# Optimization experiments

Hardware: AMD Instinct MI355X
Metric: run time of the kernel (lower is better)

## Reference

```python
import jax, jax.numpy as jnp
import numpy as np

D_MODEL = 1024
NUM_HEADS = 16
HEAD_DIM = D_MODEL // NUM_HEADS


def setup_inputs() -> dict:
    key = jax.random.key(0)
    k1, k2, k3, k4, k5 = jax.random.split(key, 5)
    scale = 1.0 / np.sqrt(D_MODEL)
    x = jax.random.normal(k1, (2, 2048, D_MODEL), dtype=jnp.float32)
    Wqkv = jax.random.uniform(k2, (D_MODEL, 3 * D_MODEL), jnp.float32, -scale, scale)
    bqkv = jax.random.uniform(k3, (3 * D_MODEL,), jnp.float32, -scale, scale)
    Wout = jax.random.uniform(k4, (D_MODEL, D_MODEL), jnp.float32, -scale, scale)
    bout = jax.random.uniform(k5, (D_MODEL,), jnp.float32, -scale, scale)
    return {"x": x, "Wqkv": Wqkv, "bqkv": bqkv, "Wout": Wout, "bout": bout}


def reference(x, Wqkv, bqkv, Wout, bout):
    B, S, _ = x.shape
    qkv = x @ Wqkv + bqkv                                   # [B, S, 3*D]
    # reshape to [B, S, H, 3*head_dim] then to [B, H, S, 3*head_dim]
    qkv = qkv.reshape(B, S, NUM_HEADS, 3 * HEAD_DIM).transpose(0, 2, 1, 3)
    q, k, v = jnp.split(qkv, 3, axis=-1)                    # each [B, H, S, hd]
    scaled = jnp.einsum("bhqd,bhkd->bhqk", q, k) / jnp.sqrt(jnp.float32(HEAD_DIM))
    attn = jax.nn.softmax(scaled, axis=-1)                  # [B, H, S, S]
    values = jnp.einsum("bhqk,bhkd->bhqd", attn, v)         # [B, H, S, hd]
    values = values.transpose(0, 2, 1, 3).reshape(B, S, D_MODEL)
    return values @ Wout + bout
```

## Files before the change

kernel.cpp:

```cpp
#include <hip/hip_runtime.h>


typedef __attribute__((ext_vector_type(8)))  short short8;
typedef __attribute__((ext_vector_type(4)))  short short4v;
typedef __attribute__((ext_vector_type(8)))  float float8;
typedef __attribute__((ext_vector_type(4)))  float f32x4;
typedef __attribute__((ext_vector_type(16))) float f32x16;
typedef __attribute__((ext_vector_type(4)))  int   int4v;

#define D_MODEL 1024
#define NHEAD   16
#define HD      64
#define SEQ     2048
#define N3      (3*D_MODEL)
#define MB      (1024*1024)

static __device__ __forceinline__ float bf2f(short s) {
    unsigned u = ((unsigned)(unsigned short)s) << 16;
    return __builtin_bit_cast(float, u);
}
static __device__ __forceinline__ short f2bf(float f) {
    unsigned u = __builtin_bit_cast(unsigned, f);
    u = (u + 0x7fff + ((u >> 16) & 1)) >> 16;
    return (short)u;
}
static __device__ __forceinline__ unsigned cvtpk(float a, float b) {
    unsigned r;
    asm("v_cvt_pk_bf16_f32 %0, %1, %2" : "=v"(r) : "v"(a), "v"(b));
    return r;
}
#define PLSWAP(a, b) asm("v_permlane32_swap_b32 %0, %1" : "+v"(a), "+v"(b))

static __device__ __forceinline__ void gl16(const short* g, short* l) {
    __builtin_amdgcn_global_load_lds(
        (const __attribute__((address_space(1))) unsigned int*)g,
        (__attribute__((address_space(3))) unsigned int*)l, 16, 0, 0);
}

__global__ __launch_bounds__(256) void prep(
    const float* __restrict__ x, const float* __restrict__ Wqkv,
    const float* __restrict__ Wout,
    short* __restrict__ Xh, short* __restrict__ Xl,
    short* __restrict__ Wh, short* __restrict__ Wl,
    short* __restrict__ Woh, short* __restrict__ Wol)
{
    __shared__ float tile[32][33];
    const int bid = blockIdx.x;
    const int tid = threadIdx.x;

    if (bid < 2048) {
        const int i = (bid * 256 + tid) * 8;
        const float8 v = *(const float8*)&x[i];
        short8 h, l;
#pragma unroll
        for (int j = 0; j < 8; ++j) {
            h[j] = f2bf(v[j]);
            l[j] = f2bf(v[j] - bf2f(h[j]));
        }
        *(short8*)&Xh[i] = h;
        *(short8*)&Xl[i] = l;
        return;
    }

    const float* in; short *hi, *lo; int K, N, bx, by;
    if (bid < 5120) {
        const int b2 = bid - 2048;
        in = Wqkv; hi = Wh; lo = Wl; K = D_MODEL; N = N3;
        bx = b2 % 96; by = b2 / 96;
    } else {
        const int b3 = bid - 5120;
        in = Wout; hi = Woh; lo = Wol; K = D_MODEL; N = D_MODEL;
        bx = b3 & 31; by = b3 >> 5;
    }
    const int n0 = bx * 32, k0 = by * 32;
    const int tx = tid & 31, ty = tid >> 5;
#pragma unroll
    for (int i = 0; i < 4; ++i)
        tile[ty + 8*i][tx] = in[(k0 + ty + 8*i) * N + (n0 + tx)];
    __syncthreads();
#pragma unroll
    for (int i = 0; i < 4; ++i) {
        const float v  = tile[tx][ty + 8*i];
        const short vh = f2bf(v);
        const short vl = f2bf(v - bf2f(vh));
        const int idx  = (n0 + ty + 8*i) * K + (k0 + tx);
        hi[idx] = vh;
        lo[idx] = vl;
    }
}

#define QBUF_SH 20480
#define OFF_AL  4096
#define OFF_BH  8192
#define OFF_BL  14336

__global__ __launch_bounds__(512, 4) void qkv_gemm8(
    const short* __restrict__ Xh, const short* __restrict__ Xl,
    const short* __restrict__ Bh, const short* __restrict__ Bl,
    const float* __restrict__ bias,
    short* __restrict__ Qo, short* __restrict__ Ko, short* __restrict__ Vt)
{
    __shared__ __attribute__((aligned(16))) short smem[2 * QBUF_SH];

    const int tid  = threadIdx.x;
    const int wave = tid >> 6, lane = tid & 63;
    const int q4 = lane >> 4, l16 = lane & 15;
    const int wr = wave >> 2, wc = wave & 3;
    const int csw = (q4 ^ ((l16 ^ (l16 >> 2)) & 3)) * 8;

    const int flat = blockIdx.x;
    const int sw = (flat & 7) * 64 + (flat >> 3);
    const int mt = sw & 31, nt = sw >> 5;
    const int m0 = mt * 128, n0 = nt * 192;

    const short* srcp[5];
#pragma unroll
    for (int j = 0; j < 5; ++j) {
        const int id = j * 512 + tid;
        int r; const short* mat; int row0;
        if (id < 512)       { r = id >> 2;          mat = Xh; row0 = m0; }
        else if (id < 1024) { r = (id - 512) >> 2;  mat = Xl; row0 = m0; }
        else if (id < 1792) { r = (id - 1024) >> 2; mat = Bh; row0 = n0; }
        else                { r = (id - 1792) >> 2; mat = Bl; row0 = n0; }
        const int cg = (id & 3) ^ ((r ^ (r >> 2)) & 3);
        srcp[j] = &mat[(size_t)(row0 + r) * D_MODEL + cg * 8];
    }

    auto stage = [&](int b) {
#pragma unroll
        for (int j = 0; j < 5; ++j) {
            gl16(srcp[j], smem + b * QBUF_SH + (j * 512 + tid) * 8);
            srcp[j] += 32;
        }
    };

    f32x4 acc[4][3];
#pragma unroll
    for (int i = 0; i < 4; ++i)
#pragma unroll
        for (int j = 0; j < 3; ++j) acc[i][j] = (f32x4){0.f, 0.f, 0.f, 0.f};

    stage(0);
    asm volatile("s_waitcnt vmcnt(0)" ::: "memory");
    __builtin_amdgcn_s_barrier();

    for (int t = 0; t < 32; ++t) {
        const int cur = t & 1;
        const short* base = smem + cur * QBUF_SH;
        const short* Ah_s = base;
        const short* Al_s = base + OFF_AL;
        const short* Bh_s = base + OFF_BH;
        const short* Bl_s = base + OFF_BL;

        short8 bhf[3], blf[3], a0h[2], a0l[2];
#pragma unroll
        for (int n = 0; n < 3; ++n) {
            const int rb = (wc * 48 + n * 16 + l16) * 32 + csw;
            bhf[n] = *(const short8*)(Bh_s + rb);
            blf[n] = *(const short8*)(Bl_s + rb);
        }
#pragma unroll
        for (int ti = 0; ti < 2; ++ti) {
            const int ra = (wr * 64 + ti * 16 + l16) * 32 + csw;
            a0h[ti] = *(const short8*)(Ah_s + ra);
            a0l[ti] = *(const short8*)(Al_s + ra);
        }
        if (t < 31) stage(cur ^ 1);
        __builtin_amdgcn_s_barrier();
        asm volatile("s_waitcnt lgkmcnt(0)" ::: "memory");
        __builtin_amdgcn_sched_barrier(0);
        short8 a1h[2], a1l[2];
#pragma unroll
        for (int ti = 0; ti < 2; ++ti) {
            const int ra = (wr * 64 + (2 + ti) * 16 + l16) * 32 + csw;
            a1h[ti] = *(const short8*)(Ah_s + ra);
            a1l[ti] = *(const short8*)(Al_s + ra);
        }
        __builtin_amdgcn_sched_barrier(0);
        __builtin_amdgcn_s_setprio(1);
#pragma unroll
        for (int ti = 0; ti < 2; ++ti)
#pragma unroll
            for (int n = 0; n < 3; ++n) {
                acc[ti][n] = __builtin_amdgcn_mfma_f32_16x16x32_bf16(a0h[ti], bhf[n], acc[ti][n], 0, 0, 0);
                acc[ti][n] = __builtin_amdgcn_mfma_f32_16x16x32_bf16(a0h[ti], blf[n], acc[ti][n], 0, 0, 0);
                acc[ti][n] = __builtin_amdgcn_mfma_f32_16x16x32_bf16(a0l[ti], bhf[n], acc[ti][n], 0, 0, 0);
            }
        __builtin_amdgcn_s_setprio(0);
        __builtin_amdgcn_s_barrier();

        asm volatile("s_waitcnt lgkmcnt(0)" ::: "memory");
        __builtin_amdgcn_sched_barrier(0);
        __builtin_amdgcn_s_setprio(1);
#pragma unroll
        for (int ti = 0; ti < 2; ++ti)
#pragma unroll
            for (int n = 0; n < 3; ++n) {
                acc[2+ti][n] = __builtin_amdgcn_mfma_f32_16x16x32_bf16(a1h[ti], bhf[n], acc[2+ti][n], 0, 0, 0);
                acc[2+ti][n] = __builtin_amdgcn_mfma_f32_16x16x32_bf16(a1h[ti], blf[n], acc[2+ti][n], 0, 0, 0);
                acc[2+ti][n] = __builtin_amdgcn_mfma_f32_16x16x32_bf16(a1l[ti], bhf[n], acc[2+ti][n], 0, 0, 0);
            }
        __builtin_amdgcn_s_setprio(0);
        asm volatile("s_waitcnt vmcnt(0)" ::: "memory");
        __builtin_amdgcn_s_barrier();
    }

    const float SCALE_Q = 0.125f * 1.4426950408889634f;
#pragma unroll
    for (int tj = 0; tj < 3; ++tj) {
        const int jj = wc * 48 + tj * 16 + l16;
        const int n  = nt * 192 + jj;
        const float bv = bias[n];
#pragma unroll
        for (int ti = 0; ti < 4; ++ti) {
            const int mb = m0 + wr * 64 + ti * 16 + q4 * 4;
            const int b = mb >> 11;
            const int s = mb & 2047;
            const int bh_ = b * NHEAD + nt;
            if (jj >= 128) {
                short4v v4;
#pragma unroll
                for (int r = 0; r < 4; ++r) v4[r] = f2bf(acc[ti][tj][r] + bv);
                *(short4v*)&Vt[(bh_ * HD + (jj - 128)) * SEQ + s] = v4;
            } else if (jj < 64) {
#pragma unroll
                for (int r = 0; r < 4; ++r)
                    Qo[(bh_ * SEQ + s + r) * HD + jj] = f2bf((acc[ti][tj][r] + bv) * SCALE_Q);
            } else {
#pragma unroll
                for (int r = 0; r < 4; ++r)
                    Ko[(bh_ * SEQ + s + r) * HD + (jj - 64)] = f2bf(acc[ti][tj][r] + bv);
            }
        }
    }
}

__global__ __launch_bounds__(256, 2) void attn_tscore(
    const short* __restrict__ Q, const short* __restrict__ K,
    const short* __restrict__ Vt,
    float* __restrict__ Opart, float2* __restrict__ Ml)
{
    __shared__ __attribute__((aligned(16))) char smem[36864];
    short (*Ks)[72] = (short(*)[72])smem;
    short (*Vs)[72] = (short(*)[72])(smem + 18432);

    const int bh  = blockIdx.x;
    const int qb  = blockIdx.y;
    const int kvz = blockIdx.z;

    const short* Qp  = Q  + (size_t)bh * SEQ * HD;
    const short* Kp  = K  + (size_t)bh * SEQ * HD + (size_t)kvz * 1024 * HD;
    const short* Vtp = Vt + (size_t)bh * HD * SEQ + (size_t)kvz * 1024;

    const int tid  = threadIdx.x;
    const int wave = tid >> 6, lane = tid & 63;
    const int l5 = lane & 31, hf = lane >> 5;
    const int q0w = qb * 128 + wave * 32;

    short8 qf[4];
#pragma unroll
    for (int c = 0; c < 4; ++c)
        qf[c] = *(const short8*)&Qp[(q0w + l5) * HD + c * 16 + hf * 8];

    f32x16 oacc0 = (f32x16)(0.f), oacc1 = (f32x16)(0.f);
    float m = -1.0e30f, l = 0.f;

    const int sr = tid >> 2;
    const int sc = (tid & 3) * 16;

    short8 kr0 = *(const short8*)&Kp[sr * HD + sc];
    short8 kr1 = *(const short8*)&Kp[sr * HD + sc + 8];
    short8 vr0 = *(const short8*)&Vtp[sr * SEQ + sc];
    short8 vr1 = *(const short8*)&Vtp[sr * SEQ + sc + 8];
    *(short8*)&Ks[sr][sc]     = kr0;
    *(short8*)&Ks[sr][sc + 8] = kr1;
    *(short8*)&Vs[sr][sc]     = vr0;
    *(short8*)&Vs[sr][sc + 8] = vr1;
    __syncthreads();

    for (int kc = 0; kc < 16; ++kc) {
        const int buf = (kc & 1) << 6;

        if (kc < 15) {
            const int nkb = (kc + 1) << 6;
            kr0 = *(const short8*)&Kp[(nkb + sr) * HD + sc];
            kr1 = *(const short8*)&Kp[(nkb + sr) * HD + sc + 8];
            vr0 = *(const short8*)&Vtp[sr * SEQ + nkb + sc];
            vr1 = *(const short8*)&Vtp[sr * SEQ + nkb + sc + 8];
        }

        f32x16 s0 = (f32x16)(0.f), s1 = (f32x16)(0.f);
#pragma unroll
        for (int c = 0; c < 4; ++c) {
            const short8 ka0 = *(const short8*)&Ks[buf + l5][c * 16 + hf * 8];
            const short8 ka1 = *(const short8*)&Ks[buf + 32 + l5][c * 16 + hf * 8];
            s0 = __builtin_amdgcn_mfma_f32_32x32x16_bf16(ka0, qf[c], s0, 0, 0, 0);
            s1 = __builtin_amdgcn_mfma_f32_32x32x16_bf16(ka1, qf[c], s1, 0, 0, 0);
        }

        float t[8];
#pragma unroll
        for (int i = 0; i < 8; ++i)
            t[i] = fmaxf(fmaxf(s0[i], s0[i + 8]), fmaxf(s1[i], s1[i + 8]));
        float pmax = fmaxf(fmaxf(fmaxf(t[0], t[1]), fmaxf(t[2], t[3])),
                           fmaxf(fmaxf(t[4], t[5]), fmaxf(t[6], t[7])));
        pmax = fmaxf(pmax, __shfl_xor(pmax, 32, 64));

        if (!__all(pmax - m <= 8.0f)) {
            const float mnew  = fmaxf(m, pmax);
            const float alpha = exp2f(m - mnew);
#pragma unroll
            for (int i = 0; i < 16; ++i) { oacc0[i] *= alpha; oacc1[i] *= alpha; }
            l *= alpha;
            m = mnew;
        }

        float p0[16], p1[16];
#pragma unroll
        for (int i = 0; i < 16; ++i) { p0[i] = exp2f(s0[i] - m); p1[i] = exp2f(s1[i] - m); }
        float sa = 0.f, sb = 0.f, sc_ = 0.f, sd = 0.f;
#pragma unroll
        for (int i = 0; i < 4; ++i) {
            sa += p0[i] + p0[i + 8];
            sb += p0[i + 4] + p0[i + 12];
            sc_ += p1[i] + p1[i + 8];
            sd += p1[i + 4] + p1[i + 12];
        }
        float rs = (sa + sb) + (sc_ + sd);
        rs += __shfl_xor(rs, 32, 64);
        l += rs;

        unsigned u0 = cvtpk(p0[0],  p0[1]),  u1 = cvtpk(p0[2],  p0[3]);
        unsigned u2 = cvtpk(p0[4],  p0[5]),  u3 = cvtpk(p0[6],  p0[7]);
        unsigned u4 = cvtpk(p0[8],  p0[9]),  u5 = cvtpk(p0[10], p0[11]);
        unsigned u6 = cvtpk(p0[12], p0[13]), u7 = cvtpk(p0[14], p0[15]);
        unsigned w0 = cvtpk(p1[0],  p1[1]),  w1 = cvtpk(p1[2],  p1[3]);
        unsigned w2 = cvtpk(p1[4],  p1[5]),  w3 = cvtpk(p1[6],  p1[7]);
        unsigned w4 = cvtpk(p1[8],  p1[9]),  w5 = cvtpk(p1[10], p1[11]);
        unsigned w6 = cvtpk(p1[12], p1[13]), w7 = cvtpk(p1[14], p1[15]);
        PLSWAP(u0, u2); PLSWAP(u1, u3); PLSWAP(u4, u6); PLSWAP(u5, u7);
        PLSWAP(w0, w2); PLSWAP(w1, w3); PLSWAP(w4, w6); PLSWAP(w5, w7);
        int4v pb0 = (int4v){ (int)u0, (int)u1, (int)u2, (int)u3 };
        int4v pb1 = (int4v){ (int)u4, (int)u5, (int)u6, (int)u7 };
        int4v pb2 = (int4v){ (int)w0, (int)w1, (int)w2, (int)w3 };
        int4v pb3 = (int4v){ (int)w4, (int)w5, (int)w6, (int)w7 };
        const short8 pbf0 = __builtin_bit_cast(short8, pb0);
        const short8 pbf1 = __builtin_bit_cast(short8, pb1);
        const short8 pbf2 = __builtin_bit_cast(short8, pb2);
        const short8 pbf3 = __builtin_bit_cast(short8, pb3);

        {
            const short8 va0 = *(const short8*)&Vs[buf + l5][hf * 8];
            const short8 va1 = *(const short8*)&Vs[buf + l5][16 + hf * 8];
            const short8 va2 = *(const short8*)&Vs[buf + l5][32 + hf * 8];
            const short8 va3 = *(const short8*)&Vs[buf + l5][48 + hf * 8];
            oacc0 = __builtin_amdgcn_mfma_f32_32x32x16_bf16(va0, pbf0, oacc0, 0, 0, 0);
            oacc0 = __builtin_amdgcn_mfma_f32_32x32x16_bf16(va1, pbf1, oacc0, 0, 0, 0);
            oacc0 = __builtin_amdgcn_mfma_f32_32x32x16_bf16(va2, pbf2, oacc0, 0, 0, 0);
            oacc0 = __builtin_amdgcn_mfma_f32_32x32x16_bf16(va3, pbf3, oacc0, 0, 0, 0);
            const short8 vb0 = *(const short8*)&Vs[buf + 32 + l5][hf * 8];
            const short8 vb1 = *(const short8*)&Vs[buf + 32 + l5][16 + hf * 8];
            const short8 vb2 = *(const short8*)&Vs[buf + 32 + l5][32 + hf * 8];
            const short8 vb3 = *(const short8*)&Vs[buf + 32 + l5][48 + hf * 8];
            oacc1 = __builtin_amdgcn_mfma_f32_32x32x16_bf16(vb0, pbf0, oacc1, 0, 0, 0);
            oacc1 = __builtin_amdgcn_mfma_f32_32x32x16_bf16(vb1, pbf1, oacc1, 0, 0, 0);
            oacc1 = __builtin_amdgcn_mfma_f32_32x32x16_bf16(vb2, pbf2, oacc1, 0, 0, 0);
            oacc1 = __builtin_amdgcn_mfma_f32_32x32x16_bf16(vb3, pbf3, oacc1, 0, 0, 0);
        }

        if (kc < 15) {
            const int wb = ((kc + 1) & 1) << 6;
            *(short8*)&Ks[wb + sr][sc]     = kr0;
            *(short8*)&Ks[wb + sr][sc + 8] = kr1;
            *(short8*)&Vs[wb + sr][sc]     = vr0;
            *(short8*)&Vs[wb + sr][sc + 8] = vr1;
        }
        __syncthreads();
    }

    float* Op = Opart + ((((size_t)kvz * 32 + bh) * 16 + qb) * 4 + wave) * 2048;
#pragma unroll
    for (int r = 0; r < 4; ++r) {
        float4 v;
        v.x = oacc0[4*r]; v.y = oacc0[4*r+1]; v.z = oacc0[4*r+2]; v.w = oacc0[4*r+3];
        *(float4*)&Op[r * 256 + lane * 4] = v;
    }
#pragma unroll
    for (int r = 0; r < 4; ++r) {
        float4 v;
        v.x = oacc1[4*r]; v.y = oacc1[4*r+1]; v.z = oacc1[4*r+2]; v.w = oacc1[4*r+3];
        *(float4*)&Op[(4 + r) * 256 + lane * 4] = v;
    }
    if (hf == 0) {
        float2 mv; mv.x = m; mv.y = l;
        Ml[((size_t)kvz * 32 + bh) * 2048 + q0w + l5] = mv;
    }
}

__global__ __launch_bounds__(256) void attn_merge(
    const float* __restrict__ Opart, const float2* __restrict__ Ml,
    short* __restrict__ Ch, short* __restrict__ Cl)
{
    __shared__ float epi[4][32][68];
    const int tid = threadIdx.x, wave = tid >> 6, lane = tid & 63;
    const int l5 = lane & 31, hf = lane >> 5;
    const int task = blockIdx.x * 4 + wave;
    const int bh = task >> 6;
    const int qb = (task >> 2) & 15;
    const int wq = task & 3;
    const int bi = bh >> 4, hi_ = bh & 15;
    const int q0w = qb * 128 + wq * 32;

    const float2 v0 = Ml[(size_t)bh * 2048 + q0w + l5];
    const float2 v1 = Ml[((size_t)32 + bh) * 2048 + q0w + l5];
    const float M  = fmaxf(v0.x, v1.x);
    const float w0 = exp2f(v0.x - M), w1 = exp2f(v1.x - M);
    const float inv = 1.0f / (v0.y * w0 + v1.y * w1);
    const float f0 = w0 * inv, f1 = w1 * inv;

    const float* Op0 = Opart + (((size_t)bh * 16 + qb) * 4 + wq) * 2048;
    const float* Op1 = Opart + ((((size_t)32 + bh) * 16 + qb) * 4 + wq) * 2048;
    float o[32];
#pragma unroll
    for (int r = 0; r < 8; ++r) {
        const float4 a = *(const float4*)&Op0[r * 256 + lane * 4];
        const float4 b = *(const float4*)&Op1[r * 256 + lane * 4];
        o[4*r]   = a.x * f0 + b.x * f1;
        o[4*r+1] = a.y * f0 + b.y * f1;
        o[4*r+2] = a.z * f0 + b.z * f1;
        o[4*r+3] = a.w * f0 + b.w * f1;
    }
#pragma unroll
    for (int r = 0; r < 16; ++r) {
        const int d = (r & 3) + 8 * (r >> 2) + 4 * hf;
        epi[wave][l5][d]      = o[r];
        epi[wave][l5][32 + d] = o[16 + r];
    }
    __builtin_amdgcn_s_waitcnt(0);
#pragma unroll
    for (int pass = 0; pass < 8; ++pass) {
        const int row = pass * 4 + (lane >> 4);
        const int col = (lane & 15) * 4;
        const float4 v = *(const float4*)&epi[wave][row][col];
        const float ov[4] = {v.x, v.y, v.z, v.w};
        short4v hh, ll;
#pragma unroll
        for (int i = 0; i < 4; ++i) {
            hh[i] = f2bf(ov[i]);
            ll[i] = f2bf(ov[i] - bf2f(hh[i]));
        }
        const size_t co = ((size_t)(bi * SEQ + q0w + row)) * D_MODEL + hi_ * HD + col;
        *(short4v*)&Ch[co] = hh;
        *(short4v*)&Cl[co] = ll;
    }
}

__global__ __launch_bounds__(256) void out_gemm128(
    const short* __restrict__ Ah, const short* __restrict__ Al,
    const short* __restrict__ Bh, const short* __restrict__ Bl,
    const float* __restrict__ bias, float* __restrict__ out)
{
    __shared__ short AhS[128*32], AlS[128*32], BhS[128*32], BlS[128*32];

    const int tid  = threadIdx.x;
    const int wave = tid >> 6, lane = tid & 63;
    const int q4 = lane >> 4, l16 = lane & 15;
    const int m0 = blockIdx.y * 128, n0 = blockIdx.x * 128;
    const int rw = (wave & 1) * 64, cw = (wave >> 1) * 64;
    const int trow = tid >> 2;
    const int tcol = (((tid & 3) ^ ((trow ^ (trow >> 2)) & 3))) * 8;
    const int csw = (q4 ^ ((l16 ^ (l16 >> 2)) & 3)) * 8;

    f32x4 acc[4][4];
#pragma unroll
    for (int i = 0; i < 4; ++i)
#pragma unroll
        for (int j = 0; j < 4; ++j) acc[i][j] = (f32x4){0.f, 0.f, 0.f, 0.f};

    for (int kt = 0; kt < D_MODEL; kt += 32) {
        gl16(&Ah[(m0 + trow) * D_MODEL + kt + tcol],      AhS + tid * 8);
        gl16(&Ah[(m0 + 64 + trow) * D_MODEL + kt + tcol], AhS + 2048 + tid * 8);
        gl16(&Al[(m0 + trow) * D_MODEL + kt + tcol],      AlS + tid * 8);
        gl16(&Al[(m0 + 64 + trow) * D_MODEL + kt + tcol], AlS + 2048 + tid * 8);
        gl16(&Bh[(n0 + trow) * D_MODEL + kt + tcol],      BhS + tid * 8);
        gl16(&Bh[(n0 + 64 + trow) * D_MODEL + kt + tcol], BhS + 2048 + tid * 8);
        gl16(&Bl[(n0 + trow) * D_MODEL + kt + tcol],      BlS + tid * 8);
        gl16(&Bl[(n0 + 64 + trow) * D_MODEL + kt + tcol], BlS + 2048 + tid * 8);
        __syncthreads();

        short8 ah[4], al[4], bh[4], bl[4];
#pragma unroll
        for (int t = 0; t < 4; ++t) {
            const int ra = (rw + t * 16 + l16) * 32 + csw;
            const int rb = (cw + t * 16 + l16) * 32 + csw;
            ah[t] = *(const short8*)&AhS[ra];
            al[t] = *(const short8*)&AlS[ra];
            bh[t] = *(const short8*)&BhS[rb];
            bl[t] = *(const short8*)&BlS[rb];
        }
#pragma unroll
        for (int ti = 0; ti < 4; ++ti)
#pragma unroll
            for (int tj = 0; tj < 4; ++tj) {
                acc[ti][tj] = __builtin_amdgcn_mfma_f32_16x16x32_bf16(ah[ti], bh[tj], acc[ti][tj], 0, 0, 0);
                acc[ti][tj] = __builtin_amdgcn_mfma_f32_16x16x32_bf16(ah[ti], bl[tj], acc[ti][tj], 0, 0, 0);
                acc[ti][tj] = __builtin_amdgcn_mfma_f32_16x16x32_bf16(al[ti], bh[tj], acc[ti][tj], 0, 0, 0);
            }
        __syncthreads();
    }

#pragma unroll
    for (int tj = 0; tj < 4; ++tj) {
        const int n = n0 + cw + tj * 16 + l16;
        const float bv = bias[n];
#pragma unroll
        for (int ti = 0; ti < 4; ++ti) {
            const int mb = m0 + rw + ti * 16 + q4 * 4;
#pragma unroll
            for (int r = 0; r < 4; ++r)
                out[(mb + r) * D_MODEL + n] = acc[ti][tj][r] + bv;
        }
    }
}

extern "C" void kernel_launch(void* const* d_in, const int* in_sizes, int n_in,
                              void* d_out, int out_size, void* d_ws, size_t ws_size,
                              hipStream_t stream)
{
    const float* x    = (const float*)d_in[0];
    const float* Wqkv = (const float*)d_in[1];
    const float* bqkv = (const float*)d_in[2];
    const float* Wout = (const float*)d_in[3];
    const float* bout = (const float*)d_in[4];
    float* out = (float*)d_out;

    char* ws = (char*)d_ws;
    short*  Woh   = (short*)(ws);
    short*  Wol   = (short*)(ws +  2*MB);
    short*  Qb    = (short*)(ws +  4*MB);
    short*  Kb    = (short*)(ws + 12*MB);
    short*  Vtb   = (short*)(ws + 20*MB);
    float*  Opart = (float*)(ws + 28*MB);
    float2* Ml    = (float2*)(ws + 60*MB);
    short*  Ch    = (short*)(ws +  4*MB);
    short*  Cl    = (short*)(ws + 12*MB);
    short*  Xh    = (short*)(ws + 28*MB);
    short*  Xl    = (short*)(ws + 36*MB);
    short*  Wh    = (short*)(ws + 44*MB);
    short*  Wl    = (short*)(ws + 50*MB);

    prep<<<6144, 256, 0, stream>>>(x, Wqkv, Wout, Xh, Xl, Wh, Wl, Woh, Wol);
    qkv_gemm8<<<dim3(512), 512, 0, stream>>>(Xh, Xl, Wh, Wl, bqkv, Qb, Kb, Vtb);
    attn_tscore<<<dim3(32, 16, 2), 256, 0, stream>>>(Qb, Kb, Vtb, Opart, Ml);
    attn_merge<<<512, 256, 0, stream>>>(Opart, Ml, Ch, Cl);
    out_gemm128<<<dim3(8, 32), 256, 0, stream>>>(Ch, Cl, Woh, Wol, bout, out);
}
```

Before: 275.8 us.

## Triple-buffer QKV GEMM LDS staging with two-stage-ahead prefetch

The QKV projection GEMM moves from a double-buffered LDS ring to a triple-buffered one. Global loads are now issued two K-steps ahead, and the wait uses a partial vmcnt so one stage's loads can stay in flight. The mid-iteration barrier split of the A fragments is removed in favour of a single fragment load and one MFMA phase per step. LDS use grows to about 120 KB per block, so launch bounds drop from 4 to 2 blocks per CU, giving up occupancy for deeper latency hiding.

New measurement: 286.8 us. 4.0% more time.

```diff
diff --git a/kernel.cpp b/kernel.cpp
--- a/kernel.cpp
+++ b/kernel.cpp
@@ -94,13 +94,13 @@
 #define OFF_BH  8192
 #define OFF_BL  14336
 
-__global__ __launch_bounds__(512, 4) void qkv_gemm8(
+__global__ __launch_bounds__(512, 2) void qkv_gemm8(
     const short* __restrict__ Xh, const short* __restrict__ Xl,
     const short* __restrict__ Bh, const short* __restrict__ Bl,
     const float* __restrict__ bias,
     short* __restrict__ Qo, short* __restrict__ Ko, short* __restrict__ Vt)
 {
-    __shared__ __attribute__((aligned(16))) short smem[2 * QBUF_SH];
+    __shared__ __attribute__((aligned(16))) short smem[3 * QBUF_SH];
 
     const int tid  = threadIdx.x;
     const int wave = tid >> 6, lane = tid & 63;
@@ -141,18 +141,20 @@
         for (int j = 0; j < 3; ++j) acc[i][j] = (f32x4){0.f, 0.f, 0.f, 0.f};
 
     stage(0);
-    asm volatile("s_waitcnt vmcnt(0)" ::: "memory");
+    stage(1);
+    asm volatile("s_waitcnt vmcnt(5)" ::: "memory");
     __builtin_amdgcn_s_barrier();
 
     for (int t = 0; t < 32; ++t) {
-        const int cur = t & 1;
-        const short* base = smem + cur * QBUF_SH;
+        const short* base = smem + (t % 3) * QBUF_SH;
         const short* Ah_s = base;
         const short* Al_s = base + OFF_AL;
         const short* Bh_s = base + OFF_BH;
         const short* Bl_s = base + OFF_BL;
 
-        short8 bhf[3], blf[3], a0h[2], a0l[2];
+        if (t < 30) stage((t + 2) % 3);
+
+        short8 bhf[3], blf[3], ahf[4], alf[4];
 #pragma unroll
         for (int n = 0; n < 3; ++n) {
             const int rb = (wc * 48 + n * 16 + l16) * 32 + csw;
@@ -160,48 +162,25 @@
             blf[n] = *(const short8*)(Bl_s + rb);
         }
 #pragma unroll
-        for (int ti = 0; ti < 2; ++ti) {
+        for (int ti = 0; ti < 4; ++ti) {
             const int ra = (wr * 64 + ti * 16 + l16) * 32 + csw;
-            a0h[ti] = *(const short8*)(Ah_s + ra);
-            a0l[ti] = *(const short8*)(Al_s + ra);
-        }
-        if (t < 31) stage(cur ^ 1);
-        __builtin_amdgcn_s_barrier();
-        asm volatile("s_waitcnt lgkmcnt(0)" ::: "memory");
-        __builtin_amdgcn_sched_barrier(0);
-        short8 a1h[2], a1l[2];
-#pragma unroll
-        for (int ti = 0; ti < 2; ++ti) {
-            const int ra = (wr * 64 + (2 + ti) * 16 + l16) * 32 + csw;
-            a1h[ti] = *(const short8*)(Ah_s + ra);
-            a1l[ti] = *(const short8*)(Al_s + ra);
-        }
-        __builtin_amdgcn_sched_barrier(0);
-        __builtin_amdgcn_s_setprio(1);
-#pragma unroll
-        for (int ti = 0; ti < 2; ++ti)
-#pragma unroll
-            for (int n = 0; n < 3; ++n) {
-                acc[ti][n] = __builtin_amdgcn_mfma_f32_16x16x32_bf16(a0h[ti], bhf[n], acc[ti][n], 0, 0, 0);
-                acc[ti][n] = __builtin_amdgcn_mfma_f32_16x16x32_bf16(a0h[ti], blf[n], acc[ti][n], 0, 0, 0);
-                acc[ti][n] = __builtin_amdgcn_mfma_f32_16x16x32_bf16(a0l[ti], bhf[n], acc[ti][n], 0, 0, 0);
-            }
-        __builtin_amdgcn_s_setprio(0);
-        __builtin_amdgcn_s_barrier();
-
+            ahf[ti] = *(const short8*)(Ah_s + ra);
+            alf[ti] = *(const short8*)(Al_s + ra);
+        }
         asm volatile("s_waitcnt lgkmcnt(0)" ::: "memory");
         __builtin_amdgcn_sched_barrier(0);
         __builtin_amdgcn_s_setprio(1);
 #pragma unroll
-        for (int ti = 0; ti < 2; ++ti)
+        for (int ti = 0; ti < 4; ++ti)
 #pragma unroll
             for (int n = 0; n < 3; ++n) {
-                acc[2+ti][n] = __builtin_amdgcn_mfma_f32_16x16x32_bf16(a1h[ti], bhf[n], acc[2+ti][n], 0, 0, 0);
-                acc[2+ti][n] = __builtin_amdgcn_mfma_f32_16x16x32_bf16(a1h[ti], blf[n], acc[2+ti][n], 0, 0, 0);
-                acc[2+ti][n] = __builtin_amdgcn_mfma_f32_16x16x32_bf16(a1l[ti], bhf[n], acc[2+ti][n], 0, 0, 0);
+                acc[ti][n] = __builtin_amdgcn_mfma_f32_16x16x32_bf16(ahf[ti], bhf[n], acc[ti][n], 0, 0, 0);
+                acc[ti][n] = __builtin_amdgcn_mfma_f32_16x16x32_bf16(ahf[ti], blf[n], acc[ti][n], 0, 0, 0);
+                acc[ti][n] = __builtin_amdgcn_mfma_f32_16x16x32_bf16(alf[ti], bhf[n], acc[ti][n], 0, 0, 0);
             }
         __builtin_amdgcn_s_setprio(0);
-        asm volatile("s_waitcnt vmcnt(0)" ::: "memory");
+        if (t < 30)      asm volatile("s_waitcnt vmcnt(5)" ::: "memory");
+        else if (t == 30) asm volatile("s_waitcnt vmcnt(0)" ::: "memory");
         __builtin_amdgcn_s_barrier();
     }
 
```

## Double-buffer output projection GEMM with smaller 128x64 tiles and swizzled grid

Applied to the files above, without the earlier changes.

Replaces the single-buffered 128x128 output GEMM with a 128x64-tile kernel that double-buffers LDS, prefetching the next K slice while the current one feeds MFMAs. The grid becomes 512 blocks in a 1D launch with a remapped block order for L2 locality, and the kernel uses setprio and sched_barrier to interleave LDS reads with MFMA. This targets the under-filled 256-block launch and the exposed global-load latency, at the cost of more B-tile reloads and more complex synchronisation.

Measured after the change: 263.3 us. 4.6% less time.

```diff
diff --git a/kernel.cpp b/kernel.cpp
--- a/kernel.cpp
+++ b/kernel.cpp
@@ -455,70 +455,131 @@
     }
 }
 
-__global__ __launch_bounds__(256) void out_gemm128(
+#define OBUF_SH 12288
+#define OO_AL   4096
+#define OO_BH   8192
+#define OO_BL   10240
+
+__global__ __launch_bounds__(256, 4) void out_gemm2(
     const short* __restrict__ Ah, const short* __restrict__ Al,
     const short* __restrict__ Bh, const short* __restrict__ Bl,
     const float* __restrict__ bias, float* __restrict__ out)
 {
-    __shared__ short AhS[128*32], AlS[128*32], BhS[128*32], BlS[128*32];
+    __shared__ __attribute__((aligned(16))) short smem[2 * OBUF_SH];
 
     const int tid  = threadIdx.x;
     const int wave = tid >> 6, lane = tid & 63;
     const int q4 = lane >> 4, l16 = lane & 15;
-    const int m0 = blockIdx.y * 128, n0 = blockIdx.x * 128;
-    const int rw = (wave & 1) * 64, cw = (wave >> 1) * 64;
-    const int trow = tid >> 2;
-    const int tcol = (((tid & 3) ^ ((trow ^ (trow >> 2)) & 3))) * 8;
+    const int wr = wave >> 1, wc = wave & 1;
     const int csw = (q4 ^ ((l16 ^ (l16 >> 2)) & 3)) * 8;
 
-    f32x4 acc[4][4];
+    const int flat = blockIdx.x;
+    const int sw = (flat & 7) * 64 + (flat >> 3);
+    const int mt = sw & 31, nt = sw >> 5;
+    const int m0 = mt * 128, n0 = nt * 64;
+
+    const short* srcp[6];
+#pragma unroll
+    for (int j = 0; j < 6; ++j) {
+        const int id = j * 256 + tid;
+        int r; const short* mat; int row0;
+        if (id < 512)       { r = id >> 2;          mat = Ah; row0 = m0; }
+        else if (id < 1024) { r = (id - 512) >> 2;  mat = Al; row0 = m0; }
+        else if (id < 1280) { r = (id - 1024) >> 2; mat = Bh; row0 = n0; }
+        else                { r = (id - 1280) >> 2; mat = Bl; row0 = n0; }
+        const int cg = (id & 3) ^ ((r ^ (r >> 2)) & 3);
+        srcp[j] = &mat[(size_t)(row0 + r) * D_MODEL + cg * 8];
+    }
+
+    auto stage = [&](int b) {
+#pragma unroll
+        for (int j = 0; j < 6; ++j) {
+            gl16(srcp[j], smem + b * OBUF_SH + (j * 256 + tid) * 8);
+            srcp[j] += 32;
+        }
+    };
+
+    f32x4 acc[4][2];
 #pragma unroll
     for (int i = 0; i < 4; ++i)
 #pragma unroll
-        for (int j = 0; j < 4; ++j) acc[i][j] = (f32x4){0.f, 0.f, 0.f, 0.f};
-
-    for (int kt = 0; kt < D_MODEL; kt += 32) {
-        gl16(&Ah[(m0 + trow) * D_MODEL + kt + tcol],      AhS + tid * 8);
-        gl16(&Ah[(m0 + 64 + trow) * D_MODEL + kt + tcol], AhS + 2048 + tid * 8);
-        gl16(&Al[(m0 + trow) * D_MODEL + kt + tcol],      AlS + tid * 8);
-        gl16(&Al[(m0 + 64 + trow) * D_MODEL + kt + tcol], AlS + 2048 + tid * 8);
-        gl16(&Bh[(n0 + trow) * D_MODEL + kt + tcol],      BhS + tid * 8);
-        gl16(&Bh[(n0 + 64 + trow) * D_MODEL + kt + tcol], BhS + 2048 + tid * 8);
-        gl16(&Bl[(n0 + trow) * D_MODEL + kt + tcol],      BlS + tid * 8);
-        gl16(&Bl[(n0 + 64 + trow) * D_MODEL + kt + tcol], BlS + 2048 + tid * 8);
-        __syncthreads();
-
-        short8 ah[4], al[4], bh[4], bl[4];
-#pragma unroll
-        for (int t = 0; t < 4; ++t) {
-            const int ra = (rw + t * 16 + l16) * 32 + csw;
-            const int rb = (cw + t * 16 + l16) * 32 + csw;
-            ah[t] = *(const short8*)&AhS[ra];
-            al[t] = *(const short8*)&AlS[ra];
-            bh[t] = *(const short8*)&BhS[rb];
-            bl[t] = *(const short8*)&BlS[rb];
-        }
-#pragma unroll
-        for (int ti = 0; ti < 4; ++ti)
-#pragma unroll
-            for (int tj = 0; tj < 4; ++tj) {
-                acc[ti][tj] = __builtin_amdgcn_mfma_f32_16x16x32_bf16(ah[ti], bh[tj], acc[ti][tj], 0, 0, 0);
-                acc[ti][tj] = __builtin_amdgcn_mfma_f32_16x16x32_bf16(ah[ti], bl[tj], acc[ti][tj], 0, 0, 0);
-                acc[ti][tj] = __builtin_amdgcn_mfma_f32_16x16x32_bf16(al[ti], bh[tj], acc[ti][tj], 0, 0, 0);
+        for (int j = 0; j < 2; ++j) acc[i][j] = (f32x4){0.f, 0.f, 0.f, 0.f};
+
+    stage(0);
+    asm volatile("s_waitcnt vmcnt(0)" ::: "memory");
+    __builtin_amdgcn_s_barrier();
+
+    for (int t = 0; t < 32; ++t) {
+        const int cur = t & 1;
+        const short* base = smem + cur * OBUF_SH;
+        const short* Ah_s = base;
+        const short* Al_s = base + OO_AL;
+        const short* Bh_s = base + OO_BH;
+        const short* Bl_s = base + OO_BL;
+
+        short8 bhf[2], blf[2], a0h[2], a0l[2];
+#pragma unroll
+        for (int n = 0; n < 2; ++n) {
+            const int rb = (wc * 32 + n * 16 + l16) * 32 + csw;
+            bhf[n] = *(const short8*)(Bh_s + rb);
+            blf[n] = *(const short8*)(Bl_s + rb);
+        }
+#pragma unroll
+        for (int ti = 0; ti < 2; ++ti) {
+            const int ra = (wr * 64 + ti * 16 + l16) * 32 + csw;
+            a0h[ti] = *(const short8*)(Ah_s + ra);
+            a0l[ti] = *(const short8*)(Al_s + ra);
+        }
+        if (t < 31) stage(cur ^ 1);
+        __builtin_amdgcn_s_barrier();
+        asm volatile("s_waitcnt lgkmcnt(0)" ::: "memory");
+        __builtin_amdgcn_sched_barrier(0);
+        short8 a1h[2], a1l[2];
+#pragma unroll
+        for (int ti = 0; ti < 2; ++ti) {
+            const int ra = (wr * 64 + (2 + ti) * 16 + l16) * 32 + csw;
+            a1h[ti] = *(const short8*)(Ah_s + ra);
+            a1l[ti] = *(const short8*)(Al_s + ra);
+        }
+        __builtin_amdgcn_sched_barrier(0);
+        __builtin_amdgcn_s_setprio(1);
+#pragma unroll
+        for (int ti = 0; ti < 2; ++ti)
+#pragma unroll
+            for (int n = 0; n < 2; ++n) {
+                acc[ti][n] = __builtin_amdgcn_mfma_f32_16x16x32_bf16(a0h[ti], bhf[n], acc[ti][n], 0, 0, 0);
+                acc[ti][n] = __builtin_amdgcn_mfma_f32_16x16x32_bf16(a0h[ti], blf[n], acc[ti][n], 0, 0, 0);
+                acc[ti][n] = __builtin_amdgcn_mfma_f32_16x16x32_bf16(a0l[ti], bhf[n], acc[ti][n], 0, 0, 0);
             }
-        __syncthreads();
-    }
-
-#pragma unroll
-    for (int tj = 0; tj < 4; ++tj) {
-        const int n = n0 + cw + tj * 16 + l16;
+        __builtin_amdgcn_s_setprio(0);
+        __builtin_amdgcn_s_barrier();
+
+        asm volatile("s_waitcnt lgkmcnt(0)" ::: "memory");
+        __builtin_amdgcn_sched_barrier(0);
+        __builtin_amdgcn_s_setprio(1);
+#pragma unroll
+        for (int ti = 0; ti < 2; ++ti)
+#pragma unroll
+            for (int n = 0; n < 2; ++n) {
+                acc[2+ti][n] = __builtin_amdgcn_mfma_f32_16x16x32_bf16(a1h[ti], bhf[n], acc[2+ti][n], 0, 0, 0);
+                acc[2+ti][n] = __builtin_amdgcn_mfma_f32_16x16x32_bf16(a1h[ti], blf[n], acc[2+ti][n], 0, 0, 0);
+                acc[2+ti][n] = __builtin_amdgcn_mfma_f32_16x16x32_bf16(a1l[ti], bhf[n], acc[2+ti][n], 0, 0, 0);
+            }
+        __builtin_amdgcn_s_setprio(0);
+        asm volatile("s_waitcnt vmcnt(0)" ::: "memory");
+        __builtin_amdgcn_s_barrier();
+    }
+
+#pragma unroll
+    for (int tj = 0; tj < 2; ++tj) {
+        const int n = n0 + wc * 32 + tj * 16 + l16;
         const float bv = bias[n];
 #pragma unroll
         for (int ti = 0; ti < 4; ++ti) {
-            const int mb = m0 + rw + ti * 16 + q4 * 4;
+            const int mb = m0 + wr * 64 + ti * 16 + q4 * 4;
 #pragma unroll
             for (int r = 0; r < 4; ++r)
-                out[(mb + r) * D_MODEL + n] = acc[ti][tj][r] + bv;
+                out[(size_t)(mb + r) * D_MODEL + n] = acc[ti][tj][r] + bv;
         }
     }
 }
@@ -553,5 +614,5 @@
     qkv_gemm8<<<dim3(512), 512, 0, stream>>>(Xh, Xl, Wh, Wl, bqkv, Qb, Kb, Vtb);
     attn_tscore<<<dim3(32, 16, 2), 256, 0, stream>>>(Qb, Kb, Vtb, Opart, Ml);
     attn_merge<<<512, 256, 0, stream>>>(Opart, Ml, Ch, Cl);
-    out_gemm128<<<dim3(8, 32), 256, 0, stream>>>(Ch, Cl, Woh, Wol, bout, out);
-}
+    out_gemm2<<<dim3(512), 256, 0, stream>>>(Ch, Cl, Woh, Wol, bout, out);
+}
```
